# Performance work log

Hardware: AMD Instinct MI355X
Metric: run time of the kernel (lower is better)

## Reference

```python
import jax, jax.numpy as jnp
import numpy as np

B, N, H, W = 16, 16, 512, 512


def setup_inputs() -> dict:
    key = jax.random.key(0)
    k1, k2, k3, k4, k5, k6 = jax.random.split(key, 6)
    # binary-ish segmentation masks (float, as in torch)
    masks = (jax.random.uniform(k1, (B, N, H, W)) < 0.3).astype(jnp.float32)
    target_mask = (jax.random.uniform(k2, (B, H, W)) < 0.3).astype(jnp.float32)
    # well-formed boxes: x1<x2, y1<y2, all within [0, W)/[0, H)
    x1 = jax.random.randint(k3, (B, N), 0, W // 2)
    y1 = jax.random.randint(k4, (B, N), 0, H // 2)
    wdt = jax.random.randint(k5, (B, N), 1, W // 2)
    hgt = jax.random.randint(k6, (B, N), 1, H // 2)
    boxes = jnp.stack([x1, y1, x1 + wdt, y1 + hgt], axis=-1).astype(jnp.int32)  # (B,N,4) xyxy
    return {"masks": masks, "target_mask": target_mask, "boxes": boxes}


def _edge_features(masks, target_mask, boxes):
    # masks: (B,N,H,W) float; target_mask: (B,H,W) float; boxes: (B,N,4) int xyxy
    # target_overlap[b,n] = sum(masks[b,n] * target_mask[b])  (torch loop body, vectorized)
    overlap = jnp.einsum("bnhw,bhw->bn", masks, target_mask)

    x1, y1, x2, y2 = boxes[..., 0], boxes[..., 1], boxes[..., 2], boxes[..., 3]  # (B,N)
    rows = jnp.arange(H)  # (H,)
    cols = jnp.arange(W)  # (W,)
    # separable box-mask indicators: box_mask[b,n,h,w] = row_in[b,n,h] * col_in[b,n,w]
    row_in = ((rows[None, None, :] >= y1[..., None]) & (rows[None, None, :] < y2[..., None])).astype(masks.dtype)  # (B,N,H)
    col_in = ((cols[None, None, :] >= x1[..., None]) & (cols[None, None, :] < x2[..., None])).astype(masks.dtype)  # (B,N,W)

    # intersection = sum(box_mask * target_mask) without materializing (B,N,H,W)
    intersection = jnp.einsum("bnh,bnw,bhw->bn", row_in, col_in, target_mask)
    box_area = row_in.sum(-1) * col_in.sum(-1)              # (B,N)
    target_area = target_mask.sum((-2, -1))                 # (B,)
    union = box_area + target_area[:, None] - intersection
    iou = intersection / (union + 1e-8)

    return jnp.stack([overlap, iou], axis=-1)  # (B,N,2)


def reference(masks, target_mask, boxes):
    return _edge_features(masks, target_mask, boxes)
```

## Files before the change

### kernel.cpp

```cpp
#include <hip/hip_runtime.h>

constexpr int B = 16, N = 16, H = 512, W = 512;
constexpr int HW = H * W;
constexpr int S = 16;
constexpr int CHUNK = HW / S;
constexpr int THREADS = 256;

__global__ __launch_bounds__(THREADS) void partial_kernel(
    const float* __restrict__ masks,
    const float* __restrict__ target,
    const int*   __restrict__ boxes,
    float* __restrict__ ws)
{
    int blk = blockIdx.x;
    int n  = blk % N;
    int bs = blk / N;
    int s  = bs % S;
    int b  = bs / S;
    int bn = b * N + n;

    const int x1 = boxes[bn * 4 + 0];
    const int y1 = boxes[bn * 4 + 1];
    const int x2 = boxes[bn * 4 + 2];
    const int y2 = boxes[bn * 4 + 3];

    const float4* m4 = (const float4*)(masks + (size_t)bn * HW + (size_t)s * CHUNK);
    const float4* t4 = (const float4*)(target + (size_t)b * HW + (size_t)s * CHUNK);
    const int base_idx = s * CHUNK;

    float ov = 0.f, inter = 0.f, ts = 0.f;
    for (int i = threadIdx.x; i < CHUNK / 4; i += THREADS) {
        float4 m = m4[i];
        float4 t = t4[i];
        ov += m.x * t.x + m.y * t.y + m.z * t.z + m.w * t.w;
        ts += t.x + t.y + t.z + t.w;
        int idx = base_idx + i * 4;
        int h = idx >> 9;
        int w = idx & (W - 1);
        if (h >= y1 && h < y2) {
            if (w     >= x1 && w     < x2) inter += t.x;
            if (w + 1 >= x1 && w + 1 < x2) inter += t.y;
            if (w + 2 >= x1 && w + 2 < x2) inter += t.z;
            if (w + 3 >= x1 && w + 3 < x2) inter += t.w;
        }
    }

    for (int off = 32; off > 0; off >>= 1) {
        ov    += __shfl_down(ov, off);
        inter += __shfl_down(inter, off);
        ts    += __shfl_down(ts, off);
    }
    __shared__ float red[3][THREADS / 64];
    int wave = threadIdx.x >> 6;
    if ((threadIdx.x & 63) == 0) {
        red[0][wave] = ov;
        red[1][wave] = inter;
        red[2][wave] = ts;
    }
    __syncthreads();
    if (threadIdx.x == 0) {
        float o  = red[0][0] + red[0][1] + red[0][2] + red[0][3];
        float it = red[1][0] + red[1][1] + red[1][2] + red[1][3];
        float t  = red[2][0] + red[2][1] + red[2][2] + red[2][3];
        atomicAdd(&ws[bn], o);
        atomicAdd(&ws[B * N + bn], it);
        atomicAdd(&ws[2 * B * N + bn], t);
    }
}

__global__ __launch_bounds__(B * N) void finalize_kernel(
    const int*   __restrict__ boxes,
    const float* __restrict__ ws,
    float* __restrict__ out)
{
    int bn = threadIdx.x;
    float ov    = ws[bn];
    float inter = ws[B * N + bn];
    float tarea = ws[2 * B * N + bn];
    int x1 = boxes[bn * 4 + 0], y1 = boxes[bn * 4 + 1];
    int x2 = boxes[bn * 4 + 2], y2 = boxes[bn * 4 + 3];
    int bw = min(x2, W) - max(x1, 0); if (bw < 0) bw = 0;
    int bh = min(y2, H) - max(y1, 0); if (bh < 0) bh = 0;
    float box_area = (float)bw * (float)bh;
    float uni = box_area + tarea - inter;
    float iou = inter / (uni + 1e-8f);
    out[bn * 2 + 0] = ov;
    out[bn * 2 + 1] = iou;
}

extern "C" void kernel_launch(void* const* d_in, const int* in_sizes, int n_in,
                              void* d_out, int out_size, void* d_ws, size_t ws_size,
                              hipStream_t stream) {
    const float* masks  = (const float*)d_in[0];
    const float* target = (const float*)d_in[1];
    const int*   boxes  = (const int*)d_in[2];
    float* out = (float*)d_out;
    float* ws  = (float*)d_ws;

    hipMemsetAsync(ws, 0, 3 * B * N * sizeof(float), stream);

    partial_kernel<<<B * S * N, THREADS, 0, stream>>>(masks, target, boxes, ws);
    finalize_kernel<<<1, B * N, 0, stream>>>(boxes, ws, out);
}
```

Before: 370.4 us.

## Fuse partial reduction and finalize into one block-per-pair kernel

```diff
diff --git a/kernel.cpp b/kernel.cpp
--- a/kernel.cpp
+++ b/kernel.cpp
@@ -2,41 +2,34 @@
 
 constexpr int B = 16, N = 16, H = 512, W = 512;
 constexpr int HW = H * W;
-constexpr int S = 16;
-constexpr int CHUNK = HW / S;
-constexpr int THREADS = 256;
+constexpr int THREADS = 1024;
+constexpr int NWAVE = THREADS / 64;
 
-__global__ __launch_bounds__(THREADS) void partial_kernel(
+__global__ __launch_bounds__(THREADS) void fused_kernel(
     const float* __restrict__ masks,
     const float* __restrict__ target,
     const int*   __restrict__ boxes,
-    float* __restrict__ ws)
+    float* __restrict__ out)
 {
-    int blk = blockIdx.x;
-    int n  = blk % N;
-    int bs = blk / N;
-    int s  = bs % S;
-    int b  = bs / S;
-    int bn = b * N + n;
+    const int bn = blockIdx.x;
+    const int b  = bn >> 4;
 
     const int x1 = boxes[bn * 4 + 0];
     const int y1 = boxes[bn * 4 + 1];
     const int x2 = boxes[bn * 4 + 2];
     const int y2 = boxes[bn * 4 + 3];
 
-    const float4* m4 = (const float4*)(masks + (size_t)bn * HW + (size_t)s * CHUNK);
-    const float4* t4 = (const float4*)(target + (size_t)b * HW + (size_t)s * CHUNK);
-    const int base_idx = s * CHUNK;
+    const float4* m4 = (const float4*)(masks + (size_t)bn * HW);
+    const float4* t4 = (const float4*)(target + (size_t)b * HW);
 
     float ov = 0.f, inter = 0.f, ts = 0.f;
-    for (int i = threadIdx.x; i < CHUNK / 4; i += THREADS) {
+    for (int i = threadIdx.x; i < HW / 4; i += THREADS) {
         float4 m = m4[i];
         float4 t = t4[i];
         ov += m.x * t.x + m.y * t.y + m.z * t.z + m.w * t.w;
         ts += t.x + t.y + t.z + t.w;
-        int idx = base_idx + i * 4;
-        int h = idx >> 9;
-        int w = idx & (W - 1);
+        int h = i >> 7;
+        int w = (i & 127) << 2;
         if (h >= y1 && h < y2) {
             if (w     >= x1 && w     < x2) inter += t.x;
             if (w + 1 >= x1 && w + 1 < x2) inter += t.y;
@@ -50,8 +43,8 @@
         inter += __shfl_down(inter, off);
         ts    += __shfl_down(ts, off);
     }
-    __shared__ float red[3][THREADS / 64];
-    int wave = threadIdx.x >> 6;
+    __shared__ float red[3][NWAVE];
+    const int wave = threadIdx.x >> 6;
     if ((threadIdx.x & 63) == 0) {
         red[0][wave] = ov;
         red[1][wave] = inter;
@@ -59,33 +52,16 @@
     }
     __syncthreads();
     if (threadIdx.x == 0) {
-        float o  = red[0][0] + red[0][1] + red[0][2] + red[0][3];
-        float it = red[1][0] + red[1][1] + red[1][2] + red[1][3];
-        float t  = red[2][0] + red[2][1] + red[2][2] + red[2][3];
-        atomicAdd(&ws[bn], o);
-        atomicAdd(&ws[B * N + bn], it);
-        atomicAdd(&ws[2 * B * N + bn], t);
+        float o = 0.f, it = 0.f, t = 0.f;
+        #pragma unroll
+        for (int k = 0; k < NWAVE; ++k) { o += red[0][k]; it += red[1][k]; t += red[2][k]; }
+        int bw = min(x2, W) - max(x1, 0); if (bw < 0) bw = 0;
+        int bh = min(y2, H) - max(y1, 0); if (bh < 0) bh = 0;
+        float box_area = (float)bw * (float)bh;
+        float uni = box_area + t - it;
+        out[bn * 2 + 0] = o;
+        out[bn * 2 + 1] = it / (uni + 1e-8f);
     }
-}
-
-__global__ __launch_bounds__(B * N) void finalize_kernel(
-    const int*   __restrict__ boxes,
-    const float* __restrict__ ws,
-    float* __restrict__ out)
-{
-    int bn = threadIdx.x;
-    float ov    = ws[bn];
-    float inter = ws[B * N + bn];
-    float tarea = ws[2 * B * N + bn];
-    int x1 = boxes[bn * 4 + 0], y1 = boxes[bn * 4 + 1];
-    int x2 = boxes[bn * 4 + 2], y2 = boxes[bn * 4 + 3];
-    int bw = min(x2, W) - max(x1, 0); if (bw < 0) bw = 0;
-    int bh = min(y2, H) - max(y1, 0); if (bh < 0) bh = 0;
-    float box_area = (float)bw * (float)bh;
-    float uni = box_area + tarea - inter;
-    float iou = inter / (uni + 1e-8f);
-    out[bn * 2 + 0] = ov;
-    out[bn * 2 + 1] = iou;
 }
 
 extern "C" void kernel_launch(void* const* d_in, const int* in_sizes, int n_in,
@@ -95,10 +71,6 @@
     const float* target = (const float*)d_in[1];
     const int*   boxes  = (const int*)d_in[2];
     float* out = (float*)d_out;
-    float* ws  = (float*)d_ws;
 
-    hipMemsetAsync(ws, 0, 3 * B * N * sizeof(float), stream);
-
-    partial_kernel<<<B * S * N, THREADS, 0, stream>>>(masks, target, boxes, ws);
-    finalize_kernel<<<1, B * N, 0, stream>>>(boxes, ws, out);
+    fused_kernel<<<B * N, THREADS, 0, stream>>>(masks, target, boxes, out);
 }
```

Result: no change. 366.8 us (-1.0%).
